# Performance work log

Hardware: AMD Instinct MI355X
Metric: run time of the kernel (lower is better)

The kernel has to match this reference:

```python
import jax, jax.numpy as jnp
import numpy as np

N = 50000        # N_particles
E = 800000       # edges (avg degree 16)
SD = 32          # state_dim = 3 + 2*2 + 25
OC = 16          # message_out_channels
H = 32           # MLP hidden_channels
BN_EPS = 1e-5


def _bn(h, g, b):
    # PyG MLP default BatchNorm1d, training-mode batch stats over rows
    m = h.mean(axis=0)
    v = h.var(axis=0)
    return (h - m) * jax.lax.rsqrt(v + BN_EPS) * g + b


def _mlp3(h, w1, b1, g1, be1, w2, b2, g2, be2, w3, b3):
    # Linear -> BN -> ReLU, Linear -> BN -> ReLU, Linear
    h = jax.nn.relu(_bn(h @ w1 + b1, g1, be1))
    h = jax.nn.relu(_bn(h @ w2 + b2, g2, be2))
    return h @ w3 + b3


def setup_inputs() -> dict:
    key = jax.random.key(0)
    ks = jax.random.split(key, 16)

    def rn(k, shape):
        fan_in = shape[0] if len(shape) > 1 else shape[0]
        return jax.random.normal(k, shape, jnp.float32) / np.sqrt(fan_in)

    inp = {
        "x": jax.random.normal(ks[0], (N, SD), jnp.float32),
        "edge_attr": jax.random.normal(ks[1], (E, SD), jnp.float32),
        "edge_index": jax.random.randint(ks[2], (2, E), 0, N, jnp.int64),
        # edge-weight-generating MLP: SD -> 32 -> 32 -> SD*OC
        "msg_w1": rn(ks[3], (SD, H)), "msg_b1": jnp.zeros((H,), jnp.float32),
        "msg_g1": jnp.ones((H,), jnp.float32), "msg_be1": jnp.zeros((H,), jnp.float32),
        "msg_w2": rn(ks[4], (H, H)), "msg_b2": jnp.zeros((H,), jnp.float32),
        "msg_g2": jnp.ones((H,), jnp.float32), "msg_be2": jnp.zeros((H,), jnp.float32),
        "msg_w3": rn(ks[5], (H, SD * OC)), "msg_b3": jnp.zeros((SD * OC,), jnp.float32),
        # NNConv root weight + bias
        "root_w": rn(ks[6], (SD, OC)), "root_b": jnp.zeros((OC,), jnp.float32),
        # own_state_nn MLP: (SD+OC) -> 32 -> 32 -> SD
        "own_w1": rn(ks[7], (SD + OC, H)), "own_b1": jnp.zeros((H,), jnp.float32),
        "own_g1": jnp.ones((H,), jnp.float32), "own_be1": jnp.zeros((H,), jnp.float32),
        "own_w2": rn(ks[8], (H, H)), "own_b2": jnp.zeros((H,), jnp.float32),
        "own_g2": jnp.ones((H,), jnp.float32), "own_be2": jnp.zeros((H,), jnp.float32),
        "own_w3": rn(ks[9], (H, SD)), "own_b3": jnp.zeros((SD,), jnp.float32),
    }
    return inp


def reference(x, edge_attr, edge_index,
              msg_w1, msg_b1, msg_g1, msg_be1, msg_w2, msg_b2, msg_g2, msg_be2,
              msg_w3, msg_b3, root_w, root_b,
              own_w1, own_b1, own_g1, own_be1, own_w2, own_b2, own_g2, own_be2,
              own_w3, own_b3):
    src, dst = edge_index[0], edge_index[1]
    # per-edge weight matrices: [E, SD, OC]
    W_e = _mlp3(edge_attr, msg_w1, msg_b1, msg_g1, msg_be1,
                msg_w2, msg_b2, msg_g2, msg_be2, msg_w3, msg_b3)
    W_e = W_e.reshape(-1, SD, OC)
    # gather-matmul-scatter (NNConv, aggr='add')
    msg = jnp.einsum('ei,eio->eo', x[src], W_e)          # [E, OC]
    agg = jax.ops.segment_sum(msg, dst, num_segments=N)  # [N, OC]
    messages = agg + x @ root_w + root_b                 # root weight + bias
    combined = jnp.concatenate([x, messages], axis=-1)   # [N, SD+OC]
    new_state = _mlp3(combined, own_w1, own_b1, own_g1, own_be1,
                      own_w2, own_b2, own_g2, own_be2, own_w3, own_b3)
    return new_state
```

## Files before the change

### kernel.cpp

```cpp
#include <hip/hip_runtime.h>
#include <hip/hip_fp16.h>


#define N_NODES 50000
#define N_EDGES 800000
#define SD 32
#define OC 16
#define HID 32
#define BN_EPS 1e-5f
#define ETILES 3125
#define NTILES 196

#define OFF_STATS 0u
#define OFF_M     1024u
#define OFF_EASUM 5120u
#define OFF_DEGS  5376u
#define OFF_CURS  205376u
#define OFF_DEGD  405376u
#define OFF_CURD  605376u
#define OFF_BASES 805376u
#define OFF_BASED 1005440u
#define OFF_POSS  1205504u
#define OFF_COMBO 4405504u
#define OFF_AGG   7605504u
#define OFF_H2S   10805504u
#define OFF_MSGB  62005504u

__device__ __forceinline__ float f4get(const float4& v, int ii) {
  return ii == 0 ? v.x : ii == 1 ? v.y : ii == 2 ? v.z : v.w;
}

__device__ __forceinline__ unsigned pack2(float a, float b) {
  __half2 h = __floats2half2_rn(a, b);
  return *reinterpret_cast<unsigned*>(&h);
}
__device__ __forceinline__ void unpk8(uint4 u, float* o) {
  __half2 a = *reinterpret_cast<__half2*>(&u.x), b = *reinterpret_cast<__half2*>(&u.y);
  __half2 c = *reinterpret_cast<__half2*>(&u.z), d = *reinterpret_cast<__half2*>(&u.w);
  float2 fa = __half22float2(a), fb = __half22float2(b);
  float2 fc = __half22float2(c), fd = __half22float2(d);
  o[0] = fa.x; o[1] = fa.y; o[2] = fb.x; o[3] = fb.y;
  o[4] = fc.x; o[5] = fc.y; o[6] = fd.x; o[7] = fd.y;
}

template<int I4, int IOFF>
__device__ __forceinline__ void mv_acc(const float4* __restrict__ rp,
                                       const float* __restrict__ wlds,
                                       float z[HID]) {
#pragma unroll
  for (int i4 = 0; i4 < I4; ++i4) {
    float4 rv = rp[i4];
#pragma unroll
    for (int ii = 0; ii < 4; ++ii) {
      float s = f4get(rv, ii);
      const float* wrow = wlds + (IOFF + i4 * 4 + ii) * HID;
#pragma unroll
      for (int h4 = 0; h4 < HID / 4; ++h4) {
        float4 wv = *reinterpret_cast<const float4*>(wrow + h4 * 4);
        z[h4 * 4 + 0] = fmaf(s, wv.x, z[h4 * 4 + 0]);
        z[h4 * 4 + 1] = fmaf(s, wv.y, z[h4 * 4 + 1]);
        z[h4 * 4 + 2] = fmaf(s, wv.z, z[h4 * 4 + 2]);
        z[h4 * 4 + 3] = fmaf(s, wv.w, z[h4 * 4 + 3]);
      }
    }
  }
}

__device__ __forceinline__ void mv_reg(const float* __restrict__ v,
                                       const float* __restrict__ wlds,
                                       float z[HID]) {
#pragma unroll
  for (int h = 0; h < HID; ++h) z[h] = 0.f;
#pragma unroll
  for (int i = 0; i < HID; ++i) {
    float s = v[i];
    const float* wrow = wlds + i * HID;
#pragma unroll
    for (int h4 = 0; h4 < HID / 4; ++h4) {
      float4 wv = *reinterpret_cast<const float4*>(wrow + h4 * 4);
      z[h4 * 4 + 0] = fmaf(s, wv.x, z[h4 * 4 + 0]);
      z[h4 * 4 + 1] = fmaf(s, wv.y, z[h4 * 4 + 1]);
      z[h4 * 4 + 2] = fmaf(s, wv.z, z[h4 * 4 + 2]);
      z[h4 * 4 + 3] = fmaf(s, wv.w, z[h4 * 4 + 3]);
    }
  }
}

__device__ __forceinline__ void bn_params(const float* __restrict__ stats, int off,
                                          float cntInv, const float* __restrict__ g,
                                          const float* __restrict__ be,
                                          float* __restrict__ sc, float* __restrict__ sf) {
  if (threadIdx.x < HID) {
    int h = threadIdx.x;
    float mean = stats[off + h] * cntInv;
    float var = stats[off + HID + h] * cntInv - mean * mean;
    float s = g[h] * rsqrtf(var + BN_EPS);
    sc[h] = s;
    sf[h] = fmaf(-mean, s, be[h]);
  }
}

__device__ __forceinline__ void tile_accum(const float z[HID], float* __restrict__ tile,
                                           int h, int g, float& s, float& q) {
  int tid = threadIdx.x;
  __syncthreads();
#pragma unroll
  for (int j = 0; j < HID; ++j) tile[tid * 33 + j] = z[j];
  __syncthreads();
#pragma unroll
  for (int k = 0; k < 32; ++k) {
    float v = tile[(g * 32 + k) * 33 + h];
    s += v;
    q = fmaf(v, v, q);
  }
}

__device__ __forceinline__ void tile_finish(float* __restrict__ tile, int h, int g,
                                            float s, float q,
                                            float* __restrict__ gstats) {
  int tid = threadIdx.x;
  __syncthreads();
  tile[g * 32 + h] = s;
  tile[256 + g * 32 + h] = q;
  __syncthreads();
  if (tid < 64) {
    int hh = tid & 31;
    int base = (tid < 32) ? 0 : 256;
    float acc = 0.f;
#pragma unroll
    for (int g2 = 0; g2 < 8; ++g2) acc += tile[base + g2 * 32 + hh];
    atomicAdd(gstats + ((tid < 32) ? hh : (HID + hh)), acc);
  }
}

__global__ __launch_bounds__(256) void kH(const int* __restrict__ ei,
                                          int* __restrict__ degS, int* __restrict__ degD) {
  int e = blockIdx.x * 256 + threadIdx.x;
  atomicAdd(degS + ei[e], 1);
  atomicAdd(degD + ei[N_EDGES + e], 1);
}

__global__ __launch_bounds__(1024) void kScan(const int* __restrict__ degS, int* __restrict__ baseS,
                                              const int* __restrict__ degD, int* __restrict__ baseD) {
  __shared__ int sc[1024];
  const int* deg = (blockIdx.x == 0) ? degS : degD;
  int* base = (blockIdx.x == 0) ? baseS : baseD;
  int t = threadIdx.x;
  const int C = 49;
  int st = t * C;
  int sum = 0;
  for (int k = 0; k < C; ++k) {
    int i = st + k;
    if (i < N_NODES) sum += deg[i];
  }
  sc[t] = sum;
  __syncthreads();
  for (int s = 1; s < 1024; s <<= 1) {
    int v = (t >= s) ? sc[t - s] : 0;
    __syncthreads();
    sc[t] += v;
    __syncthreads();
  }
  int run = sc[t] - sum;
  for (int k = 0; k < C; ++k) {
    int i = st + k;
    if (i < N_NODES) { base[i] = run; run += deg[i]; }
  }
  if (t == 1023) base[N_NODES] = run;
}

__global__ __launch_bounds__(256) void kRank(const int* __restrict__ ei,
    const int* __restrict__ baseS, const int* __restrict__ baseD,
    int* __restrict__ curS, int* __restrict__ curD,
    int* __restrict__ posS, unsigned* __restrict__ combo) {
  int e = blockIdx.x * 256 + threadIdx.x;
  int s = ei[e], d = ei[N_EDGES + e];
  int rs = atomicAdd(curS + s, 1);
  int ps = baseS[s] + rs;
  posS[e] = ps;
  int rd = atomicAdd(curD + d, 1);
  combo[ps] = (unsigned)(baseD[d] + rd) | ((unsigned)(s & 15) << 27);
}

__global__ __launch_bounds__(256) void sM_edge(const float* __restrict__ ea,
                                               float* __restrict__ M,
                                               float* __restrict__ easum) {
  __shared__ float t[256 * 36];
  int tid = threadIdx.x;
  int i = tid >> 3, j4 = tid & 7;
  float a0 = 0.f, a1 = 0.f, a2 = 0.f, a3 = 0.f, cs = 0.f;
#pragma unroll 1
  for (int tb = blockIdx.x; tb < ETILES; tb += gridDim.x) {
    __syncthreads();
    const float4* src = reinterpret_cast<const float4*>(ea + (size_t)tb * (256 * SD));
#pragma unroll
    for (int u = 0; u < 8; ++u) {
      int idx = u * 256 + tid;
      float4 v = src[idx];
      *reinterpret_cast<float4*>(&t[(idx >> 3) * 36 + (idx & 7) * 4]) = v;
    }
    __syncthreads();
#pragma unroll 4
    for (int k = 0; k < 256; ++k) {
      float s = t[k * 36 + i];
      float4 v = *reinterpret_cast<const float4*>(&t[k * 36 + j4 * 4]);
      a0 = fmaf(s, v.x, a0); a1 = fmaf(s, v.y, a1);
      a2 = fmaf(s, v.z, a2); a3 = fmaf(s, v.w, a3);
      if (j4 == 0) cs += s;
    }
  }
  atomicAdd(M + i * 32 + j4 * 4 + 0, a0);
  atomicAdd(M + i * 32 + j4 * 4 + 1, a1);
  atomicAdd(M + i * 32 + j4 * 4 + 2, a2);
  atomicAdd(M + i * 32 + j4 * 4 + 3, a3);
  if (j4 == 0) atomicAdd(easum + i, cs);
}

__global__ __launch_bounds__(1024) void kBN1(const float* __restrict__ M,
                                             const float* __restrict__ easum,
                                             const float* __restrict__ w1,
                                             float* __restrict__ stats) {
  __shared__ float Ms[1024], w1s[1024], part[32 * 33];
  int tid = threadIdx.x;
  Ms[tid] = M[tid];
  w1s[tid] = w1[tid];
  __syncthreads();
  int h = tid & 31, i = tid >> 5;
  float tacc = 0.f;
#pragma unroll
  for (int j = 0; j < 32; ++j) tacc = fmaf(Ms[i * 32 + j], w1s[j * 32 + h], tacc);
  part[i * 33 + h] = w1s[i * 32 + h] * tacc;
  __syncthreads();
  if (tid < 32) {
    float sq = 0.f, sm = 0.f;
#pragma unroll
    for (int i2 = 0; i2 < 32; ++i2) {
      sq += part[i2 * 33 + tid];
      sm = fmaf(easum[i2], w1s[i2 * 32 + tid], sm);
    }
    stats[tid] = sm;
    stats[32 + tid] = sq;
  }
}

__global__ __launch_bounds__(256) void s2_edge(
    const float* __restrict__ ea, const int* __restrict__ posS,
    const float* __restrict__ w1, const float* __restrict__ w2,
    const float* __restrict__ g1, const float* __restrict__ be1,
    float* __restrict__ stats, __half* __restrict__ h2s) {
  __shared__ float w1s[SD * HID], w2s[HID * HID];
  __shared__ float sc1[HID], sf1[HID];
  __shared__ float tile[256 * 33];
  for (int f = threadIdx.x; f < SD * HID; f += 256) w1s[f] = w1[f];
  for (int f = threadIdx.x; f < HID * HID; f += 256) w2s[f] = w2[f];
  bn_params(stats, 0, 1.f / N_EDGES, g1, be1, sc1, sf1);
  int h = threadIdx.x & 31, g = threadIdx.x >> 5;
  float s = 0.f, q = 0.f;
  __syncthreads();
#pragma unroll 1
  for (int t = blockIdx.x; t < ETILES; t += gridDim.x) {
    int e = t * 256 + threadIdx.x;
    const float4* rp = reinterpret_cast<const float4*>(ea + (size_t)e * SD);
    float z1[HID];
#pragma unroll
    for (int j = 0; j < HID; ++j) z1[j] = 0.f;
    mv_acc<8, 0>(rp, w1s, z1);
#pragma unroll
    for (int i = 0; i < HID; ++i) z1[i] = fmaxf(0.f, fmaf(z1[i], sc1[i], sf1[i]));
    float z2[HID];
    mv_reg(z1, w2s, z2);
    int ps = posS[e];
    unsigned us[16];
#pragma unroll
    for (int q2 = 0; q2 < 16; ++q2) us[q2] = pack2(z2[2 * q2], z2[2 * q2 + 1]);
    uint4* hp = reinterpret_cast<uint4*>(h2s + (size_t)ps * HID);
    hp[0] = make_uint4(us[0], us[1], us[2], us[3]);
    hp[1] = make_uint4(us[4], us[5], us[6], us[7]);
    hp[2] = make_uint4(us[8], us[9], us[10], us[11]);
    hp[3] = make_uint4(us[12], us[13], us[14], us[15]);
    tile_accum(z2, tile, h, g, s, q);
  }
  tile_finish(tile, h, g, s, q, stats + 64);
}

__global__ __launch_bounds__(256) void k5_gemm(
    const float* __restrict__ x, const float* __restrict__ w3,
    const float* __restrict__ b3, const unsigned* __restrict__ combo,
    const int* __restrict__ baseS, const __half* __restrict__ h2s,
    const float* __restrict__ stats, const float* __restrict__ g2,
    const float* __restrict__ be2, __half* __restrict__ msgb) {
  __shared__ float Tl[16 * 516];
  __shared__ float xsl[16][33];
  __shared__ float xbl[256];
  __shared__ float b3s[SD * OC];
  __shared__ float sc2[HID], sf2[HID];
  __shared__ int jr[2];
  int tid = threadIdx.x;
  int n0 = blockIdx.x * 16;
  for (int f = tid; f < 16 * SD; f += 256)
    xsl[f >> 5][f & 31] = x[(size_t)n0 * SD + f];
  for (int f = tid; f < SD * OC; f += 256) b3s[f] = b3[f];
  if (tid == 0) jr[0] = baseS[n0];
  if (tid == 1) jr[1] = baseS[n0 + 16];
  bn_params(stats, 64, 1.f / N_EDGES, g2, be2, sc2, sf2);
  __syncthreads();
  {
    int nl = tid >> 4, o = tid & 15;
    float a1 = 0.f;
#pragma unroll
    for (int i = 0; i < SD; ++i) a1 = fmaf(xsl[nl][i], b3s[i * OC + o], a1);
    xbl[tid] = a1;
  }
  {
    int oH = tid & 1, hh = (tid >> 1) & 31, ng = tid >> 6;
    float acc[4][8];
#pragma unroll
    for (int k = 0; k < 4; ++k)
#pragma unroll
      for (int j = 0; j < 8; ++j) acc[k][j] = 0.f;
    const float* wbase = w3 + hh * (SD * OC) + oH * 8;
#pragma unroll
    for (int i = 0; i < SD; ++i) {
      float4 wa = *reinterpret_cast<const float4*>(wbase + i * OC);
      float4 wb = *reinterpret_cast<const float4*>(wbase + i * OC + 4);
#pragma unroll
      for (int k = 0; k < 4; ++k) {
        float xv = xsl[ng * 4 + k][i];
        acc[k][0] = fmaf(xv, wa.x, acc[k][0]);
        acc[k][1] = fmaf(xv, wa.y, acc[k][1]);
        acc[k][2] = fmaf(xv, wa.z, acc[k][2]);
        acc[k][3] = fmaf(xv, wa.w, acc[k][3]);
        acc[k][4] = fmaf(xv, wb.x, acc[k][4]);
        acc[k][5] = fmaf(xv, wb.y, acc[k][5]);
        acc[k][6] = fmaf(xv, wb.z, acc[k][6]);
        acc[k][7] = fmaf(xv, wb.w, acc[k][7]);
      }
    }
#pragma unroll
    for (int k = 0; k < 4; ++k)
#pragma unroll
      for (int jj = 0; jj < 8; ++jj)
        Tl[(ng * 4 + k) * 516 + (oH * 8 + jj) * 32 + hh] = acc[k][jj];
  }
  __syncthreads();
  int jbeg = jr[0], jend = jr[1];
  for (int j = jbeg + tid; j < jend; j += 256) {
    unsigned c = combo[j];
    int dp = (int)(c & 0x07FFFFFFu);
    int nl = (int)(c >> 27);
    const uint4* hp = reinterpret_cast<const uint4*>(h2s + (size_t)j * HID);
    uint4 u0 = hp[0], u1 = hp[1], u2 = hp[2], u3 = hp[3];
    float h2v[HID];
    unpk8(u0, h2v + 0); unpk8(u1, h2v + 8);
    unpk8(u2, h2v + 16); unpk8(u3, h2v + 24);
#pragma unroll
    for (int k = 0; k < HID; ++k) h2v[k] = fmaxf(0.f, fmaf(h2v[k], sc2[k], sf2[k]));
    float m[OC];
#pragma unroll
    for (int o = 0; o < OC; ++o) m[o] = xbl[nl * 16 + o];
#pragma unroll
    for (int o = 0; o < OC; ++o) {
      const float* tb = Tl + nl * 516 + o * 32;
      float a = m[o];
#pragma unroll
      for (int h4 = 0; h4 < 8; ++h4) {
        float4 t = *reinterpret_cast<const float4*>(tb + h4 * 4);
        a = fmaf(h2v[h4 * 4 + 0], t.x, a);
        a = fmaf(h2v[h4 * 4 + 1], t.y, a);
        a = fmaf(h2v[h4 * 4 + 2], t.z, a);
        a = fmaf(h2v[h4 * 4 + 3], t.w, a);
      }
      m[o] = a;
    }
    unsigned us[8];
#pragma unroll
    for (int q = 0; q < 8; ++q) us[q] = pack2(m[2 * q], m[2 * q + 1]);
    uint4* mp = reinterpret_cast<uint4*>(msgb + (size_t)dp * OC);
    mp[0] = make_uint4(us[0], us[1], us[2], us[3]);
    mp[1] = make_uint4(us[4], us[5], us[6], us[7]);
  }
}

__global__ __launch_bounds__(256) void k6_aggr_own(
    const int* __restrict__ baseD, const __half* __restrict__ msgb,
    const float* __restrict__ x, const float* __restrict__ rootw,
    const float* __restrict__ rootb, const float* __restrict__ ow1,
    float* __restrict__ agg, float* __restrict__ stats) {
  __shared__ float xsl[16][33];
  __shared__ float aggl[16 * 17];
  __shared__ float rws[SD * OC];
  __shared__ float ow1s[(SD + OC) * HID];
  __shared__ float zt[16 * 33];
  __shared__ float rbs[OC];
  int tid = threadIdx.x;
  int n0 = blockIdx.x * 16;
  for (int f = tid; f < 16 * SD; f += 256) xsl[f >> 5][f & 31] = x[(size_t)n0 * SD + f];
  for (int f = tid; f < SD * OC; f += 256) rws[f] = rootw[f];
  for (int f = tid; f < (SD + OC) * HID; f += 256) ow1s[f] = ow1[f];
  if (tid < OC) rbs[tid] = rootb[tid];
  __syncthreads();
  int nl = tid >> 4, o = tid & 15;
  int d = n0 + nl;
  float r = rbs[o];
#pragma unroll
  for (int i = 0; i < SD; ++i) r = fmaf(xsl[nl][i], rws[i * OC + o], r);
  int b0 = baseD[d], b1 = baseD[d + 1];
  float s = 0.f;
  for (int j = b0; j < b1; ++j) s += __half2float(msgb[(size_t)j * OC + o]);
  float val = r + s;
  agg[(size_t)d * OC + o] = val;
  aggl[nl * 17 + o] = val;
  __syncthreads();
  float za = 0.f, zb = 0.f;
#pragma unroll
  for (int i = 0; i < SD; ++i) {
    float xv = xsl[nl][i];
    za = fmaf(xv, ow1s[i * HID + o], za);
    zb = fmaf(xv, ow1s[i * HID + o + 16], zb);
  }
#pragma unroll
  for (int i = 0; i < OC; ++i) {
    float mv = aggl[nl * 17 + i];
    za = fmaf(mv, ow1s[(SD + i) * HID + o], za);
    zb = fmaf(mv, ow1s[(SD + i) * HID + o + 16], zb);
  }
  zt[nl * 33 + o] = za;
  zt[nl * 33 + o + 16] = zb;
  __syncthreads();
  if (tid < 64) {
    int h = tid & 31;
    bool issq = tid >= 32;
    float acc = 0.f;
#pragma unroll
    for (int k = 0; k < 16; ++k) {
      float v = zt[k * 33 + h];
      acc += issq ? v * v : v;
    }
    atomicAdd(stats + 128 + (issq ? 32 : 0) + h, acc);
  }
}

__global__ __launch_bounds__(256) void s2_own(
    const float* __restrict__ x, const float* __restrict__ msgs,
    const float* __restrict__ w1, const float* __restrict__ w2,
    const float* __restrict__ g1, const float* __restrict__ be1,
    float* __restrict__ stats) {
  __shared__ float w1s[(SD + OC) * HID], w2s[HID * HID];
  __shared__ float sc1[HID], sf1[HID];
  __shared__ float tile[256 * 33];
  for (int f = threadIdx.x; f < (SD + OC) * HID; f += 256) w1s[f] = w1[f];
  for (int f = threadIdx.x; f < HID * HID; f += 256) w2s[f] = w2[f];
  bn_params(stats, 128, 1.f / N_NODES, g1, be1, sc1, sf1);
  int h = threadIdx.x & 31, g = threadIdx.x >> 5;
  float s = 0.f, q = 0.f;
  __syncthreads();
#pragma unroll 1
  for (int t = blockIdx.x; t < NTILES; t += gridDim.x) {
    int n = t * 256 + threadIdx.x;
    float z2[HID];
#pragma unroll
    for (int j = 0; j < HID; ++j) z2[j] = 0.f;
    if (n < N_NODES) {
      const float4* xp = reinterpret_cast<const float4*>(x + (size_t)n * SD);
      const float4* mp = reinterpret_cast<const float4*>(msgs + (size_t)n * OC);
      float z1[HID];
#pragma unroll
      for (int j = 0; j < HID; ++j) z1[j] = 0.f;
      mv_acc<8, 0>(xp, w1s, z1);
      mv_acc<4, SD>(mp, w1s, z1);
#pragma unroll
      for (int i = 0; i < HID; ++i) z1[i] = fmaxf(0.f, fmaf(z1[i], sc1[i], sf1[i]));
      mv_reg(z1, w2s, z2);
    }
    tile_accum(z2, tile, h, g, s, q);
  }
  tile_finish(tile, h, g, s, q, stats + 192);
}

__global__ __launch_bounds__(256) void k10_own_out(
    const float* __restrict__ x, const float* __restrict__ msgs,
    const float* __restrict__ w1, const float* __restrict__ w2,
    const float* __restrict__ w3o, const float* __restrict__ b3o,
    const float* __restrict__ g1, const float* __restrict__ be1,
    const float* __restrict__ g2, const float* __restrict__ be2,
    const float* __restrict__ stats, float* __restrict__ out) {
  __shared__ float w1s[(SD + OC) * HID], w2s[HID * HID], w3s[HID * SD];
  __shared__ float sc1[HID], sf1[HID], sc2[HID], sf2[HID];
  for (int f = threadIdx.x; f < (SD + OC) * HID; f += 256) w1s[f] = w1[f];
  for (int f = threadIdx.x; f < HID * HID; f += 256) w2s[f] = w2[f];
  for (int f = threadIdx.x; f < HID * SD; f += 256) w3s[f] = w3o[f];
  bn_params(stats, 128, 1.f / N_NODES, g1, be1, sc1, sf1);
  bn_params(stats, 192, 1.f / N_NODES, g2, be2, sc2, sf2);
  __syncthreads();
  int n = blockIdx.x * 256 + threadIdx.x;
  if (n >= N_NODES) return;
  const float4* xp = reinterpret_cast<const float4*>(x + (size_t)n * SD);
  const float4* mp = reinterpret_cast<const float4*>(msgs + (size_t)n * OC);
  float z1[HID];
#pragma unroll
  for (int j = 0; j < HID; ++j) z1[j] = 0.f;
  mv_acc<8, 0>(xp, w1s, z1);
  mv_acc<4, SD>(mp, w1s, z1);
#pragma unroll
  for (int i = 0; i < HID; ++i) z1[i] = fmaxf(0.f, fmaf(z1[i], sc1[i], sf1[i]));
  float z2[HID];
  mv_reg(z1, w2s, z2);
#pragma unroll
  for (int i = 0; i < HID; ++i) z2[i] = fmaxf(0.f, fmaf(z2[i], sc2[i], sf2[i]));
  float z3[HID];
  mv_reg(z2, w3s, z3);
  float4* op = reinterpret_cast<float4*>(out + (size_t)n * SD);
#pragma unroll
  for (int j4 = 0; j4 < 8; ++j4) {
    op[j4] = make_float4(z3[j4 * 4 + 0] + b3o[j4 * 4 + 0],
                         z3[j4 * 4 + 1] + b3o[j4 * 4 + 1],
                         z3[j4 * 4 + 2] + b3o[j4 * 4 + 2],
                         z3[j4 * 4 + 3] + b3o[j4 * 4 + 3]);
  }
}

extern "C" void kernel_launch(void* const* d_in, const int* in_sizes, int n_in,
                              void* d_out, int out_size, void* d_ws, size_t ws_size,
                              hipStream_t stream) {
  const float* x    = (const float*)d_in[0];
  const float* ea   = (const float*)d_in[1];
  const int*   ei   = (const int*)d_in[2];
  const float* mw1  = (const float*)d_in[3];
  const float* mg1  = (const float*)d_in[5];
  const float* mbe1 = (const float*)d_in[6];
  const float* mw2  = (const float*)d_in[7];
  const float* mg2  = (const float*)d_in[9];
  const float* mbe2 = (const float*)d_in[10];
  const float* mw3  = (const float*)d_in[11];
  const float* mb3  = (const float*)d_in[12];
  const float* rw   = (const float*)d_in[13];
  const float* rb   = (const float*)d_in[14];
  const float* ow1  = (const float*)d_in[15];
  const float* og1  = (const float*)d_in[17];
  const float* obe1 = (const float*)d_in[18];
  const float* ow2  = (const float*)d_in[19];
  const float* og2  = (const float*)d_in[21];
  const float* obe2 = (const float*)d_in[22];
  const float* ow3  = (const float*)d_in[23];
  const float* ob3  = (const float*)d_in[24];
  float* out = (float*)d_out;

  char* ws = (char*)d_ws;
  float* stats  = (float*)(ws + OFF_STATS);
  float* M      = (float*)(ws + OFF_M);
  float* easum  = (float*)(ws + OFF_EASUM);
  int* degS     = (int*)(ws + OFF_DEGS);
  int* curS     = (int*)(ws + OFF_CURS);
  int* degD     = (int*)(ws + OFF_DEGD);
  int* curD     = (int*)(ws + OFF_CURD);
  int* baseS    = (int*)(ws + OFF_BASES);
  int* baseD    = (int*)(ws + OFF_BASED);
  int* posS     = (int*)(ws + OFF_POSS);
  unsigned* combo = (unsigned*)(ws + OFF_COMBO);
  float* agg    = (float*)(ws + OFF_AGG);
  __half* h2s   = (__half*)(ws + OFF_H2S);
  __half* msgb  = (__half*)(ws + OFF_MSGB);

  hipMemsetAsync(ws, 0, 805376, stream);

  kH<<<3125, 256, 0, stream>>>(ei, degS, degD);
  kScan<<<2, 1024, 0, stream>>>(degS, baseS, degD, baseD);
  kRank<<<3125, 256, 0, stream>>>(ei, baseS, baseD, curS, curD, posS, combo);
  sM_edge<<<1024, 256, 0, stream>>>(ea, M, easum);
  kBN1<<<1, 1024, 0, stream>>>(M, easum, mw1, stats);
  s2_edge<<<1024, 256, 0, stream>>>(ea, posS, mw1, mw2, mg1, mbe1, stats, h2s);
  k5_gemm<<<3125, 256, 0, stream>>>(x, mw3, mb3, combo, baseS, h2s,
                                    stats, mg2, mbe2, msgb);
  k6_aggr_own<<<3125, 256, 0, stream>>>(baseD, msgb, x, rw, rb, ow1, agg, stats);
  s2_own<<<NTILES, 256, 0, stream>>>(x, agg, ow1, ow2, og1, obe1, stats);
  k10_own_out<<<(N_NODES + 255) / 256, 256, 0, stream>>>(
      x, agg, ow1, ow2, ow3, ob3, og1, obe1, og2, obe2, stats, out);
}
```

Measured before the change: 853.9 us.

## Compute edge MLP layers 1-2 with split-fp16 MFMA and direct BN1 stats

Replaces the first-layer statistics path (an edge_attr Gram matrix reduced through a one-block kernel) with a pass that computes layer-1 activations on MFMA and accumulates the column sum and sum of squares directly. The second pass recomputes layer 1, applies BN and ReLU, runs layer 2 on MFMA, and writes fp16 h2 rows in src-sorted order. Inputs and weights are split into hi and lo fp16 parts and combined with extra MFMAs to stay close to fp32 accuracy. Work moves from scalar FMA loops to matrix cores and one tiny serial kernel is dropped, at the cost of reading edge_attr twice with full layer-1 compute each time and some precision risk from the fp16 splitting (layer-2 input is fp16 only).

Result: faster. 733.0 us (-14.2%).

```diff
diff --git a/kernel.cpp b/kernel.cpp
--- a/kernel.cpp
+++ b/kernel.cpp
@@ -8,12 +8,9 @@
 #define OC 16
 #define HID 32
 #define BN_EPS 1e-5f
-#define ETILES 3125
 #define NTILES 196
 
 #define OFF_STATS 0u
-#define OFF_M     1024u
-#define OFF_EASUM 5120u
 #define OFF_DEGS  5376u
 #define OFF_CURS  205376u
 #define OFF_DEGD  405376u
@@ -25,6 +22,9 @@
 #define OFF_AGG   7605504u
 #define OFF_H2S   10805504u
 #define OFF_MSGB  62005504u
+
+typedef _Float16 f16x8 __attribute__((ext_vector_type(8)));
+typedef float f32x16 __attribute__((ext_vector_type(16)));
 
 __device__ __forceinline__ float f4get(const float4& v, int ii) {
   return ii == 0 ? v.x : ii == 1 ? v.y : ii == 2 ? v.z : v.w;
@@ -182,105 +182,133 @@
   combo[ps] = (unsigned)(baseD[d] + rd) | ((unsigned)(s & 15) << 27);
 }
 
-__global__ __launch_bounds__(256) void sM_edge(const float* __restrict__ ea,
-                                               float* __restrict__ M,
-                                               float* __restrict__ easum) {
-  __shared__ float t[256 * 36];
-  int tid = threadIdx.x;
-  int i = tid >> 3, j4 = tid & 7;
-  float a0 = 0.f, a1 = 0.f, a2 = 0.f, a3 = 0.f, cs = 0.f;
-#pragma unroll 1
-  for (int tb = blockIdx.x; tb < ETILES; tb += gridDim.x) {
-    __syncthreads();
-    const float4* src = reinterpret_cast<const float4*>(ea + (size_t)tb * (256 * SD));
-#pragma unroll
-    for (int u = 0; u < 8; ++u) {
-      int idx = u * 256 + tid;
-      float4 v = src[idx];
-      *reinterpret_cast<float4*>(&t[(idx >> 3) * 36 + (idx & 7) * 4]) = v;
-    }
-    __syncthreads();
-#pragma unroll 4
-    for (int k = 0; k < 256; ++k) {
-      float s = t[k * 36 + i];
-      float4 v = *reinterpret_cast<const float4*>(&t[k * 36 + j4 * 4]);
-      a0 = fmaf(s, v.x, a0); a1 = fmaf(s, v.y, a1);
-      a2 = fmaf(s, v.z, a2); a3 = fmaf(s, v.w, a3);
-      if (j4 == 0) cs += s;
-    }
-  }
-  atomicAdd(M + i * 32 + j4 * 4 + 0, a0);
-  atomicAdd(M + i * 32 + j4 * 4 + 1, a1);
-  atomicAdd(M + i * 32 + j4 * 4 + 2, a2);
-  atomicAdd(M + i * 32 + j4 * 4 + 3, a3);
-  if (j4 == 0) atomicAdd(easum + i, cs);
-}
-
-__global__ __launch_bounds__(1024) void kBN1(const float* __restrict__ M,
-                                             const float* __restrict__ easum,
-                                             const float* __restrict__ w1,
-                                             float* __restrict__ stats) {
-  __shared__ float Ms[1024], w1s[1024], part[32 * 33];
-  int tid = threadIdx.x;
-  Ms[tid] = M[tid];
-  w1s[tid] = w1[tid];
-  __syncthreads();
-  int h = tid & 31, i = tid >> 5;
-  float tacc = 0.f;
-#pragma unroll
-  for (int j = 0; j < 32; ++j) tacc = fmaf(Ms[i * 32 + j], w1s[j * 32 + h], tacc);
-  part[i * 33 + h] = w1s[i * 32 + h] * tacc;
-  __syncthreads();
-  if (tid < 32) {
-    float sq = 0.f, sm = 0.f;
-#pragma unroll
-    for (int i2 = 0; i2 < 32; ++i2) {
-      sq += part[i2 * 33 + tid];
-      sm = fmaf(easum[i2], w1s[i2 * 32 + tid], sm);
-    }
-    stats[tid] = sm;
-    stats[32 + tid] = sq;
-  }
-}
-
-__global__ __launch_bounds__(256) void s2_edge(
+template<int PHASE>
+__global__ __launch_bounds__(256) void sE(
     const float* __restrict__ ea, const int* __restrict__ posS,
     const float* __restrict__ w1, const float* __restrict__ w2,
     const float* __restrict__ g1, const float* __restrict__ be1,
     float* __restrict__ stats, __half* __restrict__ h2s) {
-  __shared__ float w1s[SD * HID], w2s[HID * HID];
-  __shared__ float sc1[HID], sf1[HID];
-  __shared__ float tile[256 * 33];
-  for (int f = threadIdx.x; f < SD * HID; f += 256) w1s[f] = w1[f];
-  for (int f = threadIdx.x; f < HID * HID; f += 256) w2s[f] = w2[f];
-  bn_params(stats, 0, 1.f / N_EDGES, g1, be1, sc1, sf1);
-  int h = threadIdx.x & 31, g = threadIdx.x >> 5;
-  float s = 0.f, q = 0.f;
-  __syncthreads();
-#pragma unroll 1
-  for (int t = blockIdx.x; t < ETILES; t += gridDim.x) {
-    int e = t * 256 + threadIdx.x;
-    const float4* rp = reinterpret_cast<const float4*>(ea + (size_t)e * SD);
-    float z1[HID];
-#pragma unroll
-    for (int j = 0; j < HID; ++j) z1[j] = 0.f;
-    mv_acc<8, 0>(rp, w1s, z1);
-#pragma unroll
-    for (int i = 0; i < HID; ++i) z1[i] = fmaxf(0.f, fmaf(z1[i], sc1[i], sf1[i]));
-    float z2[HID];
-    mv_reg(z1, w2s, z2);
-    int ps = posS[e];
-    unsigned us[16];
-#pragma unroll
-    for (int q2 = 0; q2 < 16; ++q2) us[q2] = pack2(z2[2 * q2], z2[2 * q2 + 1]);
-    uint4* hp = reinterpret_cast<uint4*>(h2s + (size_t)ps * HID);
-    hp[0] = make_uint4(us[0], us[1], us[2], us[3]);
-    hp[1] = make_uint4(us[4], us[5], us[6], us[7]);
-    hp[2] = make_uint4(us[8], us[9], us[10], us[11]);
-    hp[3] = make_uint4(us[12], us[13], us[14], us[15]);
-    tile_accum(z2, tile, h, g, s, q);
-  }
-  tile_finish(tile, h, g, s, q, stats + 64);
+  __shared__ _Float16 xpose[4][32 * 40];
+  __shared__ float sred[4][2][32];
+  int tid = threadIdx.x;
+  int lane = tid & 63, wid = tid >> 6;
+  int lr = lane & 31, lh = lane >> 5;
+
+  f16x8 w1h[2], w1l[2], w2h[2], w2l[2];
+#pragma unroll
+  for (int kf = 0; kf < 2; ++kf) {
+#pragma unroll
+    for (int j = 0; j < 8; ++j) {
+      int k = kf * 16 + lh * 8 + j;
+      float v = w1[k * HID + lr];
+      _Float16 hi = (_Float16)v;
+      w1h[kf][j] = hi;
+      w1l[kf][j] = (_Float16)(v - (float)hi);
+      if (PHASE == 1) {
+        float u = w2[k * HID + lr];
+        _Float16 uh = (_Float16)u;
+        w2h[kf][j] = uh;
+        w2l[kf][j] = (_Float16)(u - (float)uh);
+      } else {
+        w2h[kf][j] = (_Float16)0.f;
+        w2l[kf][j] = (_Float16)0.f;
+      }
+    }
+  }
+  float sc1 = 0.f, sf1 = 0.f;
+  if (PHASE == 1) {
+    float mean = stats[lr] * (1.f / N_EDGES);
+    float var = stats[32 + lr] * (1.f / N_EDGES) - mean * mean;
+    float s = g1[lr] * rsqrtf(var + BN_EPS);
+    sc1 = s;
+    sf1 = fmaf(-mean, s, be1[lr]);
+  }
+  float ssum = 0.f, ssq = 0.f;
+  _Float16* xp = xpose[wid];
+
+  for (int t = blockIdx.x * 4 + wid; t < N_EDGES / 32; t += gridDim.x * 4) {
+    int e0 = t * 32;
+    f16x8 ah[2], al[2];
+#pragma unroll
+    for (int kf = 0; kf < 2; ++kf) {
+      const float4* p = reinterpret_cast<const float4*>(
+          ea + (size_t)(e0 + lr) * SD + kf * 16 + lh * 8);
+      float4 v0 = p[0], v1 = p[1];
+      float vv[8] = {v0.x, v0.y, v0.z, v0.w, v1.x, v1.y, v1.z, v1.w};
+#pragma unroll
+      for (int j = 0; j < 8; ++j) {
+        _Float16 hi = (_Float16)vv[j];
+        ah[kf][j] = hi;
+        al[kf][j] = (_Float16)(vv[j] - (float)hi);
+      }
+    }
+    f32x16 acc = {};
+#pragma unroll
+    for (int kf = 0; kf < 2; ++kf) {
+      acc = __builtin_amdgcn_mfma_f32_32x32x16_f16(ah[kf], w1h[kf], acc, 0, 0, 0);
+      acc = __builtin_amdgcn_mfma_f32_32x32x16_f16(al[kf], w1h[kf], acc, 0, 0, 0);
+      acc = __builtin_amdgcn_mfma_f32_32x32x16_f16(ah[kf], w1l[kf], acc, 0, 0, 0);
+    }
+    if (PHASE == 0) {
+#pragma unroll
+      for (int r = 0; r < 16; ++r) {
+        ssum += acc[r];
+        ssq = fmaf(acc[r], acc[r], ssq);
+      }
+    } else {
+#pragma unroll
+      for (int r = 0; r < 16; ++r) {
+        int row = (r & 3) + 8 * (r >> 2) + 4 * lh;
+        float h1 = fmaxf(0.f, fmaf(acc[r], sc1, sf1));
+        xp[row * 40 + lr] = (_Float16)h1;
+      }
+      __builtin_amdgcn_sched_barrier(0);
+      asm volatile("s_waitcnt lgkmcnt(0)" ::: "memory");
+      __builtin_amdgcn_sched_barrier(0);
+      f32x16 acc2 = {};
+#pragma unroll
+      for (int kf = 0; kf < 2; ++kf) {
+        f16x8 a2 = *reinterpret_cast<const f16x8*>(xp + lr * 40 + kf * 16 + lh * 8);
+        acc2 = __builtin_amdgcn_mfma_f32_32x32x16_f16(a2, w2h[kf], acc2, 0, 0, 0);
+        acc2 = __builtin_amdgcn_mfma_f32_32x32x16_f16(a2, w2l[kf], acc2, 0, 0, 0);
+      }
+#pragma unroll
+      for (int r = 0; r < 16; ++r) {
+        ssum += acc2[r];
+        ssq = fmaf(acc2[r], acc2[r], ssq);
+      }
+      __builtin_amdgcn_sched_barrier(0);
+      asm volatile("s_waitcnt lgkmcnt(0)" ::: "memory");
+      __builtin_amdgcn_sched_barrier(0);
+#pragma unroll
+      for (int r = 0; r < 16; ++r) {
+        int row = (r & 3) + 8 * (r >> 2) + 4 * lh;
+        xp[row * 40 + lr] = (_Float16)acc2[r];
+      }
+      __builtin_amdgcn_sched_barrier(0);
+      asm volatile("s_waitcnt lgkmcnt(0)" ::: "memory");
+      __builtin_amdgcn_sched_barrier(0);
+      int ps = posS[e0 + lr];
+      uint4 va = *reinterpret_cast<const uint4*>(xp + lr * 40 + lh * 16);
+      uint4 vb = *reinterpret_cast<const uint4*>(xp + lr * 40 + lh * 16 + 8);
+      __half* dst = (__half*)h2s + (size_t)ps * HID + lh * 16;
+      *reinterpret_cast<uint4*>(dst) = va;
+      *reinterpret_cast<uint4*>(dst + 8) = vb;
+      __builtin_amdgcn_sched_barrier(0);
+    }
+  }
+  ssum += __shfl_xor(ssum, 32);
+  ssq += __shfl_xor(ssq, 32);
+  if (lane < 32) {
+    sred[wid][0][lane] = ssum;
+    sred[wid][1][lane] = ssq;
+  }
+  __syncthreads();
+  if (tid < 64) {
+    int h = tid & 31, part = tid >> 5;
+    float a = sred[0][part][h] + sred[1][part][h] + sred[2][part][h] + sred[3][part][h];
+    atomicAdd(stats + (PHASE == 0 ? 0 : 64) + part * 32 + h, a);
+  }
 }
 
 __global__ __launch_bounds__(256) void k5_gemm(
@@ -546,29 +574,26 @@
   float* out = (float*)d_out;
 
   char* ws = (char*)d_ws;
-  float* stats  = (float*)(ws + OFF_STATS);
-  float* M      = (float*)(ws + OFF_M);
-  float* easum  = (float*)(ws + OFF_EASUM);
-  int* degS     = (int*)(ws + OFF_DEGS);
-  int* curS     = (int*)(ws + OFF_CURS);
-  int* degD     = (int*)(ws + OFF_DEGD);
-  int* curD     = (int*)(ws + OFF_CURD);
-  int* baseS    = (int*)(ws + OFF_BASES);
-  int* baseD    = (int*)(ws + OFF_BASED);
-  int* posS     = (int*)(ws + OFF_POSS);
+  float* stats    = (float*)(ws + OFF_STATS);
+  int* degS       = (int*)(ws + OFF_DEGS);
+  int* curS       = (int*)(ws + OFF_CURS);
+  int* degD       = (int*)(ws + OFF_DEGD);
+  int* curD       = (int*)(ws + OFF_CURD);
+  int* baseS      = (int*)(ws + OFF_BASES);
+  int* baseD      = (int*)(ws + OFF_BASED);
+  int* posS       = (int*)(ws + OFF_POSS);
   unsigned* combo = (unsigned*)(ws + OFF_COMBO);
-  float* agg    = (float*)(ws + OFF_AGG);
-  __half* h2s   = (__half*)(ws + OFF_H2S);
-  __half* msgb  = (__half*)(ws + OFF_MSGB);
+  float* agg      = (float*)(ws + OFF_AGG);
+  __half* h2s     = (__half*)(ws + OFF_H2S);
+  __half* msgb    = (__half*)(ws + OFF_MSGB);
 
   hipMemsetAsync(ws, 0, 805376, stream);
 
   kH<<<3125, 256, 0, stream>>>(ei, degS, degD);
   kScan<<<2, 1024, 0, stream>>>(degS, baseS, degD, baseD);
   kRank<<<3125, 256, 0, stream>>>(ei, baseS, baseD, curS, curD, posS, combo);
-  sM_edge<<<1024, 256, 0, stream>>>(ea, M, easum);
-  kBN1<<<1, 1024, 0, stream>>>(M, easum, mw1, stats);
-  s2_edge<<<1024, 256, 0, stream>>>(ea, posS, mw1, mw2, mg1, mbe1, stats, h2s);
+  sE<0><<<1024, 256, 0, stream>>>(ea, posS, mw1, mw2, mg1, mbe1, stats, h2s);
+  sE<1><<<1024, 256, 0, stream>>>(ea, posS, mw1, mw2, mg1, mbe1, stats, h2s);
   k5_gemm<<<3125, 256, 0, stream>>>(x, mw3, mb3, combo, baseS, h2s,
                                     stats, mg2, mbe2, msgb);
   k6_aggr_own<<<3125, 256, 0, stream>>>(baseD, msgb, x, rw, rb, ow1, agg, stats);
```
